# Performance work log

Measured on AMD Instinct MI355X. Metric: run time of the kernel, lower is better.

The kernel has to match this reference:

```python
import jax, jax.numpy as jnp
import numpy as np
from jax.scipy.special import logsumexp

TEMPERATURE = 0.1
BETA = 0.999
EPS = 1e-8
HARD_K = 10  # min(num_classes // 4, 10) with num_classes = 1000


def _l2norm(x, axis=-1):
    return x * jax.lax.rsqrt(jnp.sum(x * x, axis=axis, keepdims=True) + 1e-24)


def setup_inputs() -> dict:
    key = jax.random.key(0)
    k1, k2, k3, k4, k5 = jax.random.split(key, 5)
    B, D, C, M = 4096, 1024, 1000, 32768
    return {
        "image_features": jax.random.normal(k1, (B, D), dtype=jnp.float32),
        "prompts": jax.random.normal(k2, (C, D), dtype=jnp.float32),
        "labels": jax.random.randint(k3, (B, C), 0, 2, dtype=jnp.int32),
        "memory_features": jax.random.normal(k4, (M, D), dtype=jnp.float32),
        "memory_labels": jax.random.randint(k5, (M, C), 0, 2, dtype=jnp.int32),
        "mem_ptr": 16384,
    }


def reference(image_features, prompts, labels, memory_features, memory_labels, mem_ptr):
    B, D = image_features.shape
    C = prompts.shape[0]
    labels_f = labels.astype(jnp.float32)

    # z_img = F.normalize(image_features)
    z_img = _l2norm(image_features, axis=1)

    # class weights (effective-number reweighting), computed from this batch's labels
    counts = labels_f.sum(axis=0)                              # [C]
    effective_num = 1.0 - jnp.power(jnp.float32(BETA), counts)
    weights = (1.0 - BETA) / (effective_num + EPS)
    weights = weights / jnp.sum(weights) * C                   # [C]

    # memory bank update (detached write of current batch at ptr), then use [:ptr+B]
    mem_f = memory_features.at[mem_ptr:mem_ptr + B].set(jax.lax.stop_gradient(z_img))
    mem_l = memory_labels.at[mem_ptr:mem_ptr + B].set(labels)
    used = mem_ptr + B  # static

    enhanced_features = jnp.concatenate([z_img, mem_f[:used]], axis=0)     # [N, D]
    enhanced_labels = jnp.concatenate([labels_f, mem_l[:used].astype(jnp.float32)], axis=0)  # [N, C]

    z_prompts = _l2norm(prompts, axis=1)                       # [C, D]
    sim = (enhanced_features @ z_prompts.T) / TEMPERATURE      # [N, C]

    pos_mask = enhanced_labels > 0                             # [N, C]

    # hard negatives: top-K similarities among negatives define the keep threshold
    sim_for_neg = jnp.where(pos_mask, -jnp.inf, sim)
    hard_neg_vals, _ = jax.lax.top_k(sim_for_neg, HARD_K)      # [N, K]
    min_hard_neg = hard_neg_vals[:, -1:]                       # [N, 1]
    neg_mask = (~pos_mask) & (sim >= min_hard_neg)
    full_mask = pos_mask | neg_mask

    lse = logsumexp(jnp.where(full_mask, sim, -jnp.inf), axis=1)  # [N]
    log_prob = sim - lse[:, None]                              # [N, C]

    posf = pos_mask.astype(sim.dtype)
    pos_w = posf * weights[None, :]                            # [N, C]
    weight_sums = pos_w.sum(axis=1)                            # [N]
    loss_num = (pos_w * (-log_prob)).sum(axis=1)               # [N]

    valid = weight_sums > 0
    loss_per_sample = jnp.where(valid, loss_num / (weight_sums + EPS), 0.0)
    n_valid = jnp.maximum(valid.sum(), 1)
    attr_loss = loss_per_sample.sum() / n_valid.astype(sim.dtype)
    # single attribute -> total_loss / num_valid_attrs == attr_loss
    return attr_loss
```

## Files before the change

kernel.cpp:

```cpp
#include <hip/hip_runtime.h>
#include <math.h>

#define BN    4096
#define DD    1024
#define CC    1000
#define MM    32768
#define ROWS_CAP 32768
#define SIMLD 1024

typedef __attribute__((ext_vector_type(8))) int   int8v;
typedef __attribute__((ext_vector_type(16))) float f32x16;

__device__ __forceinline__ float wave_max_f(float v) {
#pragma unroll
  for (int off = 32; off >= 1; off >>= 1) v = fmaxf(v, __shfl_xor(v, off, 64));
  return v;
}
__device__ __forceinline__ float wave_sum_f(float v) {
#pragma unroll
  for (int off = 32; off >= 1; off >>= 1) v += __shfl_xor(v, off, 64);
  return v;
}

__device__ __forceinline__ short f2bf(float f) {
  union { float f; unsigned u; } v; v.f = f;
  unsigned r = v.u + 0x7FFF + ((v.u >> 16) & 1);
  return (short)(r >> 16);
}
__device__ __forceinline__ float bf2f(unsigned short u) {
  union { unsigned u; float f; } v; v.u = ((unsigned)u) << 16;
  return v.f;
}

__device__ __forceinline__ void gload16(const unsigned char* g, unsigned char* l) {
  __builtin_amdgcn_global_load_lds(
      (const __attribute__((address_space(1))) unsigned int*)g,
      (__attribute__((address_space(3))) unsigned int*)l, 16, 0, 0);
}

__global__ __launch_bounds__(256) void count_kernel(const int* __restrict__ labels,
                                                    int* __restrict__ counts) {
  const int c = blockIdx.x * 256 + threadIdx.x;
  if (c >= CC) return;
  const int b0 = blockIdx.y * 64;
  int s = 0;
  for (int b = b0; b < b0 + 64; ++b) s += labels[(size_t)b * CC + c];
  atomicAdd(&counts[c], s);
}

__global__ __launch_bounds__(1024) void weights_kernel(const int* __restrict__ counts,
                                                       float* __restrict__ weights) {
  const int t = threadIdx.x;
  float w = 0.f;
  if (t < CC) {
    float cnt = (float)counts[t];
    float en = 1.0f - expf(cnt * logf(0.999f));
    w = (1.0f - 0.999f) / (en + 1e-8f);
  }
  float s = wave_sum_f(w);
  __shared__ float part[16];
  if ((t & 63) == 0) part[t >> 6] = s;
  __syncthreads();
  float tot = 0.f;
#pragma unroll
  for (int i = 0; i < 16; ++i) tot += part[i];
  if (t < CC) weights[t] = w * ((float)CC / tot);
}

__global__ __launch_bounds__(256) void conv_kernel(const float* __restrict__ img,
                                                   const float* __restrict__ prompts,
                                                   const float* __restrict__ mem,
                                                   const int* __restrict__ memptr,
                                                   unsigned char* __restrict__ A,
                                                   unsigned char* __restrict__ B) {
  __shared__ float part[4];
  const int t = threadIdx.x;
  const int blk = blockIdx.x;
  if (blk >= ROWS_CAP) {
    const int row = blk - ROWS_CAP;
    int packed = 0;
    if (row < CC) {
      float4 v = ((const float4*)(prompts + (size_t)row * DD))[t];
      float s = v.x * v.x + v.y * v.y + v.z * v.z + v.w * v.w;
      s = wave_sum_f(s);
      if ((t & 63) == 0) part[t >> 6] = s;
      __syncthreads();
      float sc = 10.0f * rsqrtf(part[0] + part[1] + part[2] + part[3] + 1e-24f);
      packed = __builtin_amdgcn_cvt_pk_fp8_f32(v.x * sc, v.y * sc, 0, false);
      packed = __builtin_amdgcn_cvt_pk_fp8_f32(v.z * sc, v.w * sc, packed, true);
    }
    ((int*)(B + (size_t)row * DD))[t] = packed;
    return;
  }
  const int nrows = BN + memptr[0];
  const int padded = (nrows + 127) & ~127;
  const int row = blk;
  if (row >= padded) return;
  int packed = 0;
  if (row < nrows) {
    const float* src = (row < BN) ? img + (size_t)row * DD
                                  : mem + (size_t)(row - BN) * DD;
    float4 v = ((const float4*)src)[t];
    float sc = 1.0f;
    if (row < BN) {
      float s = v.x * v.x + v.y * v.y + v.z * v.z + v.w * v.w;
      s = wave_sum_f(s);
      if ((t & 63) == 0) part[t >> 6] = s;
      __syncthreads();
      sc = rsqrtf(part[0] + part[1] + part[2] + part[3] + 1e-24f);
    }
    packed = __builtin_amdgcn_cvt_pk_fp8_f32(v.x * sc, v.y * sc, 0, false);
    packed = __builtin_amdgcn_cvt_pk_fp8_f32(v.z * sc, v.w * sc, packed, true);
  }
  ((int*)(A + (size_t)row * DD))[t] = packed;
}

__global__ __launch_bounds__(256) void gemm_mx(const unsigned char* __restrict__ A,
                                               const unsigned char* __restrict__ Bm,
                                               const int* __restrict__ memptr,
                                               short* __restrict__ simbf, int lo) {
  const int f = blockIdx.x;
  const int x = f & 7;
  const int s = f >> 3;
  const int c = s & 7;
  const int rt = (s >> 3) * 8 + x;

  const int nrows = BN + memptr[0];
  const int row0 = rt * 128;
  if (lo + row0 >= nrows) return;
  const int c0 = c * 128;

  __shared__ unsigned char As[16384];
  __shared__ unsigned char Bs[16384];

  const int t = threadIdx.x;
  const int lane = t & 63;
  const int wid = t >> 6;
  const int wm = (wid >> 1) * 64;
  const int wn = (wid & 1) * 64;

  const int r_st = t & 127;
  const int kc_hi = t >> 7;
  const unsigned char* gaB = A + (size_t)(lo + row0 + r_st) * DD;
  const unsigned char* gbB = Bm + (size_t)(c0 + r_st) * DD;
  unsigned char* lA = As + t * 16;
  unsigned char* lB = Bs + t * 16;

  f32x16 acc[2][2] = {};
  const int q = lane >> 5;
  const int rr = lane & 31;

  for (int k0 = 0; k0 < DD; k0 += 128) {
#pragma unroll
    for (int p = 0; p < 4; ++p)
      gload16(gaB + k0 + (p * 2 + kc_hi) * 16, lA + p * 4096);
#pragma unroll
    for (int p = 0; p < 4; ++p)
      gload16(gbB + k0 + (p * 2 + kc_hi) * 16, lB + p * 4096);
    __syncthreads();
#pragma unroll
    for (int h = 0; h < 2; ++h) {
      int8v af[2], bfv[2];
      const int kc = h * 4 + q * 2;
#pragma unroll
      for (int mi = 0; mi < 2; ++mi) {
        const unsigned char* pa = As + kc * 2048 + (wm + mi * 32 + rr) * 16;
        int4 lo4 = *(const int4*)pa;
        int4 hi4 = *(const int4*)(pa + 2048);
        af[mi][0] = lo4.x; af[mi][1] = lo4.y; af[mi][2] = lo4.z; af[mi][3] = lo4.w;
        af[mi][4] = hi4.x; af[mi][5] = hi4.y; af[mi][6] = hi4.z; af[mi][7] = hi4.w;
      }
#pragma unroll
      for (int ni = 0; ni < 2; ++ni) {
        const unsigned char* pb = Bs + kc * 2048 + (wn + ni * 32 + rr) * 16;
        int4 lo4 = *(const int4*)pb;
        int4 hi4 = *(const int4*)(pb + 2048);
        bfv[ni][0] = lo4.x; bfv[ni][1] = lo4.y; bfv[ni][2] = lo4.z; bfv[ni][3] = lo4.w;
        bfv[ni][4] = hi4.x; bfv[ni][5] = hi4.y; bfv[ni][6] = hi4.z; bfv[ni][7] = hi4.w;
      }
#pragma unroll
      for (int mi = 0; mi < 2; ++mi)
#pragma unroll
        for (int ni = 0; ni < 2; ++ni)
          acc[mi][ni] = __builtin_amdgcn_mfma_scale_f32_32x32x64_f8f6f4(
              af[mi], bfv[ni], acc[mi][ni], 0, 0, 0, 127, 0, 127);
    }
    __syncthreads();
  }

  const int cl = lane & 31;
  const int r4 = 4 * (lane >> 5);
#pragma unroll
  for (int mi = 0; mi < 2; ++mi)
#pragma unroll
    for (int ni = 0; ni < 2; ++ni) {
      f32x16 v = acc[mi][ni];
      const int colg = c0 + wn + ni * 32 + cl;
      const int rbase = row0 + wm + mi * 32 + r4;
#pragma unroll
      for (int reg = 0; reg < 16; ++reg) {
        const int rowl = rbase + (reg & 3) + 8 * (reg >> 2);
        simbf[(size_t)rowl * SIMLD + colg] = f2bf(v[reg]);
      }
    }
}

__global__ __launch_bounds__(256) void rowpost_kernel(
    const short* __restrict__ simbf, const int* __restrict__ labels,
    const int* __restrict__ mlabels, const float* __restrict__ weights,
    const int* __restrict__ memptr, float* __restrict__ lps_arr,
    float* __restrict__ valid_arr, int chunk_lo) {
  __shared__ float wlds[1024];
  {
    const int t = threadIdx.x;
#pragma unroll
    for (int i = 0; i < 4; ++i) {
      int c = t + i * 256;
      wlds[c] = (c < CC) ? weights[c] : 0.f;
    }
  }
  __syncthreads();

  const int nrows = BN + memptr[0];
  const int wid = threadIdx.x >> 6;
  const int lane = threadIdx.x & 63;
  const int row = chunk_lo + blockIdx.x * 4 + wid;
  if (row >= ROWS_CAP) return;
  if (row >= nrows) {
    if (lane == 0) { lps_arr[row] = 0.f; valid_arr[row] = 0.f; }
    return;
  }

  const unsigned short* srow = (const unsigned short*)simbf + (size_t)(row - chunk_lo) * SIMLD;
  const int* lrow = (row < BN) ? labels + (size_t)row * CC
                               : mlabels + (size_t)(row - BN) * CC;
  const int cbase = lane * 16;

  unsigned short sraw[16];
  *(ulonglong2*)&sraw[0] = *(const ulonglong2*)(srow + cbase);
  *(ulonglong2*)&sraw[8] = *(const ulonglong2*)(srow + cbase + 8);
  int lab[16];
#pragma unroll
  for (int g = 0; g < 4; ++g) {
    int c = cbase + g * 4;
    if (c + 3 < CC) {
      *(int4*)&lab[g * 4] = *(const int4*)(lrow + c);
    } else {
#pragma unroll
      for (int u = 0; u < 4; ++u) lab[g * 4 + u] = (c + u < CC) ? lrow[c + u] : 0;
    }
  }

  float sv[16];
  bool pv[16];
  float vneg[16];
#pragma unroll
  for (int j = 0; j < 16; ++j) {
    int c = cbase + j;
    bool ok = (c < CC);
    float sf = bf2f(sraw[j]);
    bool p = ok && (lab[j] > 0);
    sv[j] = ok ? sf : -INFINITY;
    pv[j] = p;
    vneg[j] = (ok && !p) ? sf : -INFINITY;
  }

  float v10 = -INFINITY;
  for (int r = 0; r < 10; ++r) {
    float lmx = -INFINITY;
#pragma unroll
    for (int j = 0; j < 16; ++j) lmx = fmaxf(lmx, vneg[j]);
    lmx = wave_max_f(lmx);
#pragma unroll
    for (int j = 0; j < 16; ++j) if (vneg[j] == lmx) vneg[j] = -INFINITY;
    v10 = lmx;
  }

  float mmax = -INFINITY;
#pragma unroll
  for (int j = 0; j < 16; ++j) {
    if (pv[j] || sv[j] >= v10) mmax = fmaxf(mmax, sv[j]);
  }
  mmax = wave_max_f(mmax);

  float esum = 0.f, wsum = 0.f, wsim = 0.f;
#pragma unroll
  for (int j = 0; j < 16; ++j) {
    int c = cbase + j;
    if (c < CC) {
      if (pv[j] || sv[j] >= v10) esum += expf(sv[j] - mmax);
      if (pv[j]) { float w = wlds[c]; wsum += w; wsim += w * sv[j]; }
    }
  }
  esum = wave_sum_f(esum);
  wsum = wave_sum_f(wsum);
  wsim = wave_sum_f(wsim);

  if (lane == 0) {
    float lse = mmax + logf(esum);
    bool valid = (wsum > 0.f);
    float lps = valid ? (wsum * lse - wsim) / (wsum + 1e-8f) : 0.f;
    float mult = (row < BN) ? 2.f : 1.f;
    lps_arr[row] = mult * lps;
    valid_arr[row] = valid ? mult : 0.f;
  }
}

__global__ __launch_bounds__(1024) void reduce_kernel(const float* __restrict__ lps_arr,
                                                      const float* __restrict__ valid_arr,
                                                      float* __restrict__ out) {
  const int t = threadIdx.x;
  const float4* l4 = (const float4*)lps_arr;
  const float4* v4 = (const float4*)valid_arr;
  float s1 = 0.f, s2 = 0.f;
#pragma unroll
  for (int i = 0; i < 8; ++i) {
    float4 a = l4[t + i * 1024];
    float4 b = v4[t + i * 1024];
    s1 += a.x + a.y + a.z + a.w;
    s2 += b.x + b.y + b.z + b.w;
  }
  s1 = wave_sum_f(s1);
  s2 = wave_sum_f(s2);
  __shared__ float p1[16], p2[16];
  if ((t & 63) == 0) { p1[t >> 6] = s1; p2[t >> 6] = s2; }
  __syncthreads();
  if (t == 0) {
    float a = 0.f, b = 0.f;
#pragma unroll
    for (int i = 0; i < 16; ++i) { a += p1[i]; b += p2[i]; }
    out[0] = a / fmaxf(b, 1.0f);
  }
}

extern "C" void kernel_launch(void* const* d_in, const int* in_sizes, int n_in,
                              void* d_out, int out_size, void* d_ws, size_t ws_size,
                              hipStream_t stream) {
  const float* img     = (const float*)d_in[0];
  const float* prompts = (const float*)d_in[1];
  const int*   labels  = (const int*)d_in[2];
  const float* mem     = (const float*)d_in[3];
  const int*   mlabels = (const int*)d_in[4];
  const int*   memptr  = (const int*)d_in[5];
  float* out = (float*)d_out;
  char* ws = (char*)d_ws;

  int*   counts  = (int*)(ws + 0);
  float* weights = (float*)(ws + 4096);
  float* lps_arr = (float*)(ws + 8192);
  float* val_arr = (float*)(ws + 139264);
  unsigned char* Bf8 = (unsigned char*)(ws + 270336);
  unsigned char* Af8 = (unsigned char*)(ws + 1318912);
  const size_t fixed = 1318912 + (size_t)ROWS_CAP * DD;
  short* simbf = (short*)(ws + fixed);

  long long avail = (long long)ws_size - (long long)fixed;
  int chunk = (int)(avail / (SIMLD * 2));
  chunk &= ~1023;
  if (chunk < 1024) chunk = 1024;
  if (chunk > ROWS_CAP) chunk = ROWS_CAP;

  hipMemsetAsync(ws, 0, 4096, stream);

  conv_kernel<<<ROWS_CAP + 1024, 256, 0, stream>>>(img, prompts, mem, memptr, Af8, Bf8);
  count_kernel<<<dim3((CC + 255) / 256, BN / 64), 256, 0, stream>>>(labels, counts);
  weights_kernel<<<1, 1024, 0, stream>>>(counts, weights);

  for (int lo = 0; lo < ROWS_CAP; lo += chunk) {
    int rows = (ROWS_CAP - lo < chunk) ? (ROWS_CAP - lo) : chunk;
    int rowTiles = rows / 128;
    gemm_mx<<<8 * rowTiles, 256, 0, stream>>>(Af8, Bf8, memptr, simbf, lo);
    rowpost_kernel<<<rows / 4, 256, 0, stream>>>(simbf, labels, mlabels, weights, memptr,
                                                 lps_arr, val_arr, lo);
  }
  reduce_kernel<<<1, 1024, 0, stream>>>(lps_arr, val_arr, out);
}
```

Baseline: 352.5 us.

## Pre-tile FP8 operands so GEMM tile loads are contiguous; one wave per row conversion

The conversion kernel now writes the FP8 A and B matrices in a tiled layout: 128-row blocks, with each 16-byte K chunk stored contiguously across the 128 rows. This lets the GEMM's global-to-LDS loads read one contiguous 4 KB span per pass instead of strided 16-byte pieces from 128 different rows. Conversion also switches to one wave per row with 64-byte-per-lane loads, which removes the shared-memory reduction and the block barrier. The count kernel is split into twice as many blocks with an unrolled inner loop; the cost is more atomics on the counts.

```diff
diff --git a/kernel.cpp b/kernel.cpp
--- a/kernel.cpp
+++ b/kernel.cpp
@@ -8,6 +8,7 @@
 #define ROWS_CAP 32768
 #define SIMLD 1024
 
+
 typedef __attribute__((ext_vector_type(8))) int   int8v;
 typedef __attribute__((ext_vector_type(16))) float f32x16;
 
@@ -32,6 +33,12 @@
   return v.f;
 }
 
+__device__ __forceinline__ int pack4(float a, float b, float c, float d) {
+  int p = __builtin_amdgcn_cvt_pk_fp8_f32(a, b, 0, false);
+  p = __builtin_amdgcn_cvt_pk_fp8_f32(c, d, p, true);
+  return p;
+}
+
 __device__ __forceinline__ void gload16(const unsigned char* g, unsigned char* l) {
   __builtin_amdgcn_global_load_lds(
       (const __attribute__((address_space(1))) unsigned int*)g,
@@ -42,9 +49,10 @@
                                                     int* __restrict__ counts) {
   const int c = blockIdx.x * 256 + threadIdx.x;
   if (c >= CC) return;
-  const int b0 = blockIdx.y * 64;
+  const int b0 = blockIdx.y * 32;
   int s = 0;
-  for (int b = b0; b < b0 + 64; ++b) s += labels[(size_t)b * CC + c];
+#pragma unroll
+  for (int b = 0; b < 32; ++b) s += labels[(size_t)(b0 + b) * CC + c];
   atomicAdd(&counts[c], s);
 }
 
@@ -73,46 +81,53 @@
                                                    const int* __restrict__ memptr,
                                                    unsigned char* __restrict__ A,
                                                    unsigned char* __restrict__ B) {
-  __shared__ float part[4];
   const int t = threadIdx.x;
-  const int blk = blockIdx.x;
-  if (blk >= ROWS_CAP) {
-    const int row = blk - ROWS_CAP;
-    int packed = 0;
+  const int lane = t & 63;
+  const int gr = blockIdx.x * 4 + (t >> 6);
+
+  const float* src = nullptr;
+  unsigned char* dst;
+  float extraScale = 1.0f;
+  bool needNorm = false;
+
+  if (gr >= ROWS_CAP) {
+    const int row = gr - ROWS_CAP;
+    dst = B + (size_t)(row >> 7) * 131072 + (size_t)(row & 127) * 16;
     if (row < CC) {
-      float4 v = ((const float4*)(prompts + (size_t)row * DD))[t];
-      float s = v.x * v.x + v.y * v.y + v.z * v.z + v.w * v.w;
-      s = wave_sum_f(s);
-      if ((t & 63) == 0) part[t >> 6] = s;
-      __syncthreads();
-      float sc = 10.0f * rsqrtf(part[0] + part[1] + part[2] + part[3] + 1e-24f);
-      packed = __builtin_amdgcn_cvt_pk_fp8_f32(v.x * sc, v.y * sc, 0, false);
-      packed = __builtin_amdgcn_cvt_pk_fp8_f32(v.z * sc, v.w * sc, packed, true);
-    }
-    ((int*)(B + (size_t)row * DD))[t] = packed;
-    return;
-  }
-  const int nrows = BN + memptr[0];
-  const int padded = (nrows + 127) & ~127;
-  const int row = blk;
-  if (row >= padded) return;
-  int packed = 0;
-  if (row < nrows) {
-    const float* src = (row < BN) ? img + (size_t)row * DD
-                                  : mem + (size_t)(row - BN) * DD;
-    float4 v = ((const float4*)src)[t];
-    float sc = 1.0f;
-    if (row < BN) {
-      float s = v.x * v.x + v.y * v.y + v.z * v.z + v.w * v.w;
-      s = wave_sum_f(s);
-      if ((t & 63) == 0) part[t >> 6] = s;
-      __syncthreads();
-      sc = rsqrtf(part[0] + part[1] + part[2] + part[3] + 1e-24f);
-    }
-    packed = __builtin_amdgcn_cvt_pk_fp8_f32(v.x * sc, v.y * sc, 0, false);
-    packed = __builtin_amdgcn_cvt_pk_fp8_f32(v.z * sc, v.w * sc, packed, true);
-  }
-  ((int*)(A + (size_t)row * DD))[t] = packed;
+      src = prompts + (size_t)row * DD;
+      needNorm = true;
+      extraScale = 10.0f;
+    }
+  } else {
+    const int nrows = BN + memptr[0];
+    const int padded = (nrows + 127) & ~127;
+    if (gr >= padded) return;
+    dst = A + (size_t)(gr >> 7) * 131072 + (size_t)(gr & 127) * 16;
+    if (gr < nrows) {
+      if (gr < BN) { src = img + (size_t)gr * DD; needNorm = true; }
+      else         { src = mem + (size_t)(gr - BN) * DD; }
+    }
+  }
+
+  int4 o = {0, 0, 0, 0};
+  if (src) {
+    const float4* s4 = (const float4*)src + lane * 4;
+    float4 a = s4[0], b = s4[1], c = s4[2], d = s4[3];
+    float sc = extraScale;
+    if (needNorm) {
+      float ss = a.x * a.x + a.y * a.y + a.z * a.z + a.w * a.w
+               + b.x * b.x + b.y * b.y + b.z * b.z + b.w * b.w
+               + c.x * c.x + c.y * c.y + c.z * c.z + c.w * c.w
+               + d.x * d.x + d.y * d.y + d.z * d.z + d.w * d.w;
+      ss = wave_sum_f(ss);
+      sc = extraScale * rsqrtf(ss + 1e-24f);
+    }
+    o.x = pack4(a.x * sc, a.y * sc, a.z * sc, a.w * sc);
+    o.y = pack4(b.x * sc, b.y * sc, b.z * sc, b.w * sc);
+    o.z = pack4(c.x * sc, c.y * sc, c.z * sc, c.w * sc);
+    o.w = pack4(d.x * sc, d.y * sc, d.z * sc, d.w * sc);
+  }
+  *(int4*)(dst + (size_t)lane * 2048) = o;
 }
 
 __global__ __launch_bounds__(256) void gemm_mx(const unsigned char* __restrict__ A,
@@ -139,10 +154,8 @@
   const int wm = (wid >> 1) * 64;
   const int wn = (wid & 1) * 64;
 
-  const int r_st = t & 127;
-  const int kc_hi = t >> 7;
-  const unsigned char* gaB = A + (size_t)(lo + row0 + r_st) * DD;
-  const unsigned char* gbB = Bm + (size_t)(c0 + r_st) * DD;
+  const unsigned char* gaT = A + (size_t)(lo + row0) * DD;
+  const unsigned char* gbT = Bm + (size_t)c0 * DD;
   unsigned char* lA = As + t * 16;
   unsigned char* lB = Bs + t * 16;
 
@@ -151,12 +164,13 @@
   const int rr = lane & 31;
 
   for (int k0 = 0; k0 < DD; k0 += 128) {
+    const size_t kb = (size_t)k0 * 128;
 #pragma unroll
     for (int p = 0; p < 4; ++p)
-      gload16(gaB + k0 + (p * 2 + kc_hi) * 16, lA + p * 4096);
+      gload16(gaT + kb + p * 4096 + t * 16, lA + p * 4096);
 #pragma unroll
     for (int p = 0; p < 4; ++p)
-      gload16(gbB + k0 + (p * 2 + kc_hi) * 16, lB + p * 4096);
+      gload16(gbT + kb + p * 4096 + t * 16, lB + p * 4096);
     __syncthreads();
 #pragma unroll
     for (int h = 0; h < 2; ++h) {
@@ -362,8 +376,8 @@
 
   hipMemsetAsync(ws, 0, 4096, stream);
 
-  conv_kernel<<<ROWS_CAP + 1024, 256, 0, stream>>>(img, prompts, mem, memptr, Af8, Bf8);
-  count_kernel<<<dim3((CC + 255) / 256, BN / 64), 256, 0, stream>>>(labels, counts);
+  conv_kernel<<<(ROWS_CAP + 1024) / 4, 256, 0, stream>>>(img, prompts, mem, memptr, Af8, Bf8);
+  count_kernel<<<dim3((CC + 255) / 256, BN / 32), 256, 0, stream>>>(labels, counts);
   weights_kernel<<<1, 1024, 0, stream>>>(counts, weights);
 
   for (int lo = 0; lo < ROWS_CAP; lo += chunk) {
```

After: 342.4 us. 2.9% less time.
